# Kernel tuning notes

Measured on AMD Instinct MI355X. Metric: run time of the kernel, lower is better.

## Reference

```python
import jax, jax.numpy as jnp
import numpy as np

V, E, H, B, T = 32000, 512, 1024, 16, 256


def setup_inputs() -> dict:
    key = jax.random.key(0)
    ks = jax.random.split(key, 12)
    s = 0.05
    return {
        "x": jax.random.randint(ks[0], (B, T), 0, V),
        "emb": jax.random.normal(ks[1], (V, E), jnp.float32) * s,
        "Wx0": jax.random.normal(ks[2], (E, 3 * H), jnp.float32) * s,
        "Wh0": jax.random.normal(ks[3], (H, 3 * H), jnp.float32) * s,
        "bx0": jnp.zeros((3 * H,), jnp.float32),
        "bh0": jnp.zeros((3 * H,), jnp.float32),
        "Wx1": jax.random.normal(ks[4], (H, 3 * H), jnp.float32) * s,
        "Wh1": jax.random.normal(ks[5], (H, 3 * H), jnp.float32) * s,
        "bx1": jnp.zeros((3 * H,), jnp.float32),
        "bh1": jnp.zeros((3 * H,), jnp.float32),
        "fcW": jax.random.normal(ks[6], (H, V), jnp.float32) * s,
        "fcb": jnp.zeros((V,), jnp.float32),
    }


def _gru_cell(x_t, h, Wx, Wh, bx, bh):
    # standard torch.nn.GRUCell math
    gx = x_t @ Wx + bx            # [B, 3H]
    gh = h @ Wh + bh              # [B, 3H]
    xr, xz, xn = jnp.split(gx, 3, axis=-1)
    hr, hz, hn = jnp.split(gh, 3, axis=-1)
    r = jax.nn.sigmoid(xr + hr)
    z = jax.nn.sigmoid(xz + hz)
    n = jnp.tanh(xn + r * hn)
    return (1.0 - z) * n + z * h


def reference(x, emb, Wx0, Wh0, bx0, bh0, Wx1, Wh1, bx1, bh1, fcW, fcb):
    embedded = emb[x]                       # [B, T, E]
    xs = jnp.swapaxes(embedded, 0, 1)       # [T, B, E] for scan over time
    h0_init = jnp.zeros((x.shape[0], H), embedded.dtype)

    def step(h0, x_t):
        h0_new = _gru_cell(x_t, h0, Wx0, Wh0, bx0, bh0)
        # NOTE: original code passes h_prev = new_hidden[-1] (== layer-0 output)
        # as both input and previous hidden for layer 1. Reproduced faithfully.
        h1_new = _gru_cell(h0_new, h0_new, Wx1, Wh1, bx1, bh1)
        return h0_new, (h0_new, h1_new)

    h0_final, (h0_seq, h1_seq) = jax.lax.scan(step, h0_init, xs)
    out_seq = jnp.swapaxes(h1_seq, 0, 1)    # [B, T, H] (top-layer outputs)
    logits = out_seq @ fcW + fcb            # [B, T, V]
    h1_final = h1_seq[-1]
    hidden = jnp.stack([h0_final, h1_final], axis=0)  # [2, B, H]
    return logits, hidden
```

## Files before the change

kernel.cpp:

```cpp
#include <hip/hip_runtime.h>
#include <hip/hip_bf16.h>

#define V_  32000
#define E_  512
#define H_  1024
#define B_  16
#define T_  256
#define H3  3072

#define AGENT_LD(p)    __hip_atomic_load((p),  __ATOMIC_RELAXED, __HIP_MEMORY_SCOPE_AGENT)
#define AGENT_ST(p, v) __hip_atomic_store((p), (v), __ATOMIC_RELAXED, __HIP_MEMORY_SCOPE_AGENT)

typedef __attribute__((ext_vector_type(8))) _Float16 f16x8;
typedef __attribute__((ext_vector_type(4))) float f32x4;

#define GLDS16(gp, lp) __builtin_amdgcn_global_load_lds( \
    (const __attribute__((address_space(1))) unsigned int*)(gp), \
    (__attribute__((address_space(3))) unsigned int*)(lp), 16, 0, 0)

__global__ __launch_bounds__(128) void k_embed_f16(const int* __restrict__ x,
                                                   const float* __restrict__ emb,
                                                   _Float16* __restrict__ ef) {
  const int rin = blockIdx.x;
  const int b = rin >> 8, t = rin & 255;
  const int orow = t * 16 + b;
  const int idx = x[rin];
  const float4 v = ((const float4*)(emb + (size_t)idx * E_))[threadIdx.x];
  _Float16 o[4] = {(_Float16)v.x, (_Float16)v.y, (_Float16)v.z, (_Float16)v.w};
  ushort4 u;
  u.x = *(unsigned short*)&o[0]; u.y = *(unsigned short*)&o[1];
  u.z = *(unsigned short*)&o[2]; u.w = *(unsigned short*)&o[3];
  ((ushort4*)(ef + (size_t)orow * E_))[threadIdx.x] = u;
}

__global__ __launch_bounds__(256) void k_transpose_f16(const float* __restrict__ W, int ldw,
                                                       _Float16* __restrict__ WT, int R) {
  __shared__ float tile[32][33];
  const int c0 = blockIdx.x * 32, r0 = blockIdx.y * 32;
  const int tx = threadIdx.x & 31, ty = threadIdx.x >> 5;
  #pragma unroll
  for (int i = ty; i < 32; i += 8)
    tile[i][tx] = W[(size_t)(r0 + i) * ldw + c0 + tx];
  __syncthreads();
  #pragma unroll
  for (int i = ty; i < 32; i += 8)
    WT[(size_t)(c0 + i) * R + r0 + tx] = (_Float16)tile[tx][i];
}

__global__ __launch_bounds__(512) void k_catbias(const float* __restrict__ a,
                                                 const float* __restrict__ b,
                                                 float* __restrict__ o) {
  const int i = blockIdx.x * 512 + threadIdx.x;
  o[i] = (i < H3) ? a[i] : b[i - H3];
}

__global__ __launch_bounds__(256, 4) void k_gemm_f16(
    const _Float16* __restrict__ A, const _Float16* __restrict__ BT,
    const float* __restrict__ bias, void* __restrict__ Cv,
    int MT, int NT, int K, int ldc, int remap, int cfp16) {
  __shared__ _Float16 sA[128 * 64], sB[128 * 64];

  const int bid = blockIdx.x;
  const int GROUPM = 8;
  const int group = bid / (GROUPM * NT);
  const int first = group * GROUPM;
  const int gsm = (MT - first < GROUPM) ? (MT - first) : GROUPM;
  const int rem = bid % (GROUPM * NT);
  const int pm = first + rem % gsm;
  const int pn = rem / gsm;
  const int bm = pm * 128, bn = pn * 128;

  const int tid = threadIdx.x;
  const int wv = tid >> 6, l = tid & 63;
  const int wr = wv >> 1, wc = wv & 1;
  const int frow = l & 15;
  const int ksl  = l >> 4;

  f32x4 acc[4][4];
  #pragma unroll
  for (int a = 0; a < 4; ++a)
    #pragma unroll
    for (int b = 0; b < 4; ++b) acc[a][b] = (f32x4){0.f, 0.f, 0.f, 0.f};

  for (int k0 = 0; k0 < K; k0 += 64) {
    __syncthreads();
    #pragma unroll
    for (int p = 0; p < 4; ++p) {
      const int obase = ((p << 2) + wv) << 10;
      const int row = ((obase >> 7)) + (l >> 3);
      const int slot = l & 7;
      const int gcol = k0 + ((slot ^ (row & 7)) << 3);
      GLDS16(A + (size_t)(bm + row) * K + gcol, (char*)sA + obase);
      GLDS16(BT + (size_t)(bn + row) * K + gcol, (char*)sB + obase);
    }
    __syncthreads();
    #pragma unroll
    for (int kk = 0; kk < 2; ++kk) {
      f16x8 a[4], b[4];
      #pragma unroll
      for (int f = 0; f < 4; ++f) {
        const int ar = wr * 64 + f * 16 + frow;
        a[f] = *(const f16x8*)((const char*)sA + ar * 128 + ((((kk << 2) + ksl) ^ (ar & 7)) << 4));
        const int br_ = wc * 64 + f * 16 + frow;
        b[f] = *(const f16x8*)((const char*)sB + br_ * 128 + ((((kk << 2) + ksl) ^ (br_ & 7)) << 4));
      }
      #pragma unroll
      for (int fm = 0; fm < 4; ++fm)
        #pragma unroll
        for (int fn = 0; fn < 4; ++fn)
          acc[fm][fn] = __builtin_amdgcn_mfma_f32_16x16x32_f16(a[fm], b[fn], acc[fm][fn], 0, 0, 0);
    }
  }

  const int crow0 = bm + wr * 64 + (l >> 4) * 4;
  const int ccol0 = bn + wc * 64 + (l & 15);
  #pragma unroll
  for (int fn = 0; fn < 4; ++fn) {
    const int col = ccol0 + fn * 16;
    const float bv = bias[col];
    #pragma unroll
    for (int fm = 0; fm < 4; ++fm) {
      const int r0 = crow0 + fm * 16;
      #pragma unroll
      for (int i = 0; i < 4; ++i) {
        const int rr = r0 + i;
        const int orow = remap ? ((rr & 15) * T_ + (rr >> 4)) : rr;
        const float val = acc[fm][fn][i] + bv;
        if (cfp16) ((_Float16*)Cv)[(size_t)orow * ldc + col] = (_Float16)val;
        else       ((float*)Cv)[(size_t)orow * ldc + col] = val;
      }
    }
  }
}

__global__ __launch_bounds__(512, 1) void k_recur3(
    const _Float16* __restrict__ WhTf,
    const float* __restrict__ GX0,
    const float* __restrict__ bh0,
    _Float16* __restrict__ H0f,
    float* __restrict__ H0last,
    unsigned* __restrict__ bar,
    const float* __restrict__ Wx1,
    const float* __restrict__ Wh1,
    _Float16* __restrict__ BTf) {
  __shared__ float red[12288];
  const int tid = threadIdx.x;
  const int wg = blockIdx.x;

  if (wg >= 32) {
    float* tile = red;
    const int ty = tid >> 5, tx = tid & 31;
    for (int tix = wg - 32; tix < 6144; tix += 224) {
      const int job = tix >= 3072;
      const int tt = job ? tix - 3072 : tix;
      const int c0 = (tt % 96) * 32, r0 = (tt / 96) * 32;
      const float* W = job ? Wh1 : Wx1;
      _Float16* D = BTf + (job ? (size_t)H3 * H_ : 0);
      __syncthreads();
      tile[ty * 33 + tx]        = W[(size_t)(r0 + ty) * H3 + c0 + tx];
      tile[(ty + 16) * 33 + tx] = W[(size_t)(r0 + ty + 16) * H3 + c0 + tx];
      __syncthreads();
      #pragma unroll
      for (int s = 0; s < 2; ++s) {
        const int i = ty + s * 16;
        D[(size_t)(c0 + i) * H_ + r0 + tx] = (_Float16)tile[tx * 33 + i];
      }
    }
    return;
  }

  const int rank = wg;
  const int wv = tid >> 6, l = tid & 63;
  const int b  = tid >> 5, jj = tid & 31;
  const int col = rank * 32 + jj;

  f16x8 breg[6][4];
  #pragma unroll
  for (int nf = 0; nf < 6; ++nf) {
    const int g = nf >> 1, h2 = nf & 1;
    const int bcol = g * 1024 + rank * 32 + h2 * 16 + (l & 15);
    #pragma unroll
    for (int kf = 0; kf < 4; ++kf)
      breg[nf][kf] = *(const f16x8*)(WhTf + (size_t)bcol * 1024 + wv * 128 + kf * 32 + ((l >> 4) << 3));
  }
  const float bhr = bh0[col], bhz = bh0[1024 + col], bhn = bh0[2048 + col];

  float xr, xz, xn;
  {
    const size_t g0 = (size_t)(0 * 16 + b) * H3;
    xr = GX0[g0 + col]; xz = GX0[g0 + 1024 + col]; xn = GX0[g0 + 2048 + col];
  }
  float hprev = 0.f;

  for (int t = 0; t < T_; ++t) {
    f16x8 af[4];
    if (t == 0) {
      #pragma unroll
      for (int kf = 0; kf < 4; ++kf)
        af[kf] = (f16x8){0, 0, 0, 0, 0, 0, 0, 0};
    } else {
      const unsigned* tp = &bar[(unsigned)((4 * wv + (l & 3)) * 32 + rank) * 32];
      int guard = 0;
      for (;;) {
        const unsigned v = AGENT_LD(tp);
        if (__all(v >= (unsigned)t)) break;
        if (++guard > 10000000) break;
      }
      const char* ab = (const char*)H0f + (size_t)(t - 1) * 32768 + ((l & 15) * 2048)
                       + ((wv * 128 + ((l >> 4) << 3)) << 1);
      #pragma unroll
      for (int kf = 0; kf < 4; ++kf)
        asm volatile("global_load_dwordx4 %0, %1, off sc0 sc1" : "=v"(af[kf]) : "v"(ab + kf * 64));
      asm volatile("s_waitcnt vmcnt(0)" ::: "memory");
      __builtin_amdgcn_sched_barrier(0);
    }

    #pragma unroll
    for (int nf = 0; nf < 6; ++nf) {
      f32x4 a4 = (f32x4){0.f, 0.f, 0.f, 0.f};
      #pragma unroll
      for (int kf = 0; kf < 4; ++kf)
        a4 = __builtin_amdgcn_mfma_f32_16x16x32_f16(af[kf], breg[nf][kf], a4, 0, 0, 0);
      *(f32x4*)&red[(((wv * 6 + nf) << 6) + l) << 2] = a4;
    }
    __syncthreads();

    const int h2 = jj >> 4, f = jj & 15;
    const int lp = ((b >> 2) << 4) + f, ii = b & 3;
    float p3[3];
    #pragma unroll
    for (int g = 0; g < 3; ++g) {
      const int nf = g * 2 + h2;
      float s = 0.f;
      #pragma unroll
      for (int w8 = 0; w8 < 8; ++w8)
        s += red[((((w8 * 6 + nf) << 6) + lp) << 2) + ii];
      p3[g] = s;
    }
    const float r = 1.f / (1.f + expf(-(xr + p3[0] + bhr)));
    const float z = 1.f / (1.f + expf(-(xz + p3[1] + bhz)));
    const float n = tanhf(xn + r * (p3[2] + bhn));
    const float hnew = (1.f - z) * n + z * hprev;
    hprev = hnew;

    {
      const _Float16 hf = (_Float16)hnew;
      const unsigned tmp = (unsigned)*(const unsigned short*)&hf;
      const unsigned nb = __shfl_xor(tmp, 1);
      if ((jj & 1) == 0) {
        const unsigned w = (tmp & 0xffffu) | (nb << 16);
        const size_t u32i = (((size_t)(t * 16 + b) << 10) + col) >> 1;
        AGENT_ST((unsigned*)H0f + u32i, w);
      }
    }
    if (t == T_ - 1) H0last[(b << 10) + col] = hnew;

    if (t + 1 < T_) {
      __syncthreads();
      if (tid < 32) AGENT_ST(&bar[(unsigned)(rank * 32 + tid) * 32], (unsigned)(t + 1));
      {
        const size_t g0 = (size_t)((t + 1) * 16 + b) * H3;
        xr = GX0[g0 + col]; xz = GX0[g0 + 1024 + col]; xn = GX0[g0 + 2048 + col];
      }
    }
  }
}

__global__ __launch_bounds__(256) void k_gru1(const _Float16* __restrict__ G1f,
                                              const _Float16* __restrict__ H0f,
                                              _Float16* __restrict__ H1f,
                                              float* __restrict__ H1last, int row0) {
  const int lrow = blockIdx.x;
  const int row = row0 + lrow;
  const _Float16* g = G1f + (size_t)lrow * 6144;
  for (int j = threadIdx.x; j < H_; j += 256) {
    const float xr = (float)g[j], xz = (float)g[1024 + j], xn = (float)g[2048 + j];
    const float hr = (float)g[3072 + j], hz = (float)g[4096 + j], hn = (float)g[5120 + j];
    const size_t idx = ((size_t)row << 10) + j;
    const float h = (float)H0f[idx];
    const float r = 1.f / (1.f + expf(-(xr + hr)));
    const float z = 1.f / (1.f + expf(-(xz + hz)));
    const float n = tanhf(xn + r * hn);
    const float hnew = (1.f - z) * n + z * h;
    H1f[idx] = (_Float16)hnew;
    if (row >= 4080) H1last[((row - 4080) << 10) + j] = hnew;
  }
}

__global__ __launch_bounds__(256) void k_hidden(const float* __restrict__ H0last,
                                                const float* __restrict__ H1last,
                                                float* __restrict__ out) {
  const int i = blockIdx.x * 256 + threadIdx.x;
  const int l = i >> 14;
  const int bj = i & 16383;
  out[i] = l ? H1last[bj] : H0last[bj];
}

extern "C" void kernel_launch(void* const* d_in, const int* in_sizes, int n_in,
                              void* d_out, int out_size, void* d_ws, size_t ws_size,
                              hipStream_t stream) {
  const int*   x   = (const int*)d_in[0];
  const float* emb = (const float*)d_in[1];
  const float* Wx0 = (const float*)d_in[2];
  const float* Wh0 = (const float*)d_in[3];
  const float* bx0 = (const float*)d_in[4];
  const float* bh0 = (const float*)d_in[5];
  const float* Wx1 = (const float*)d_in[6];
  const float* Wh1 = (const float*)d_in[7];
  const float* bx1 = (const float*)d_in[8];
  const float* bh1 = (const float*)d_in[9];
  const float* fcW = (const float*)d_in[10];
  const float* fcb = (const float*)d_in[11];
  float* out = (float*)d_out;

  char* ws = (char*)d_ws;
  const size_t MB = 1024 * 1024;
  _Float16* H0f    = (_Float16*)(ws + 0);
  _Float16* H1f    = (_Float16*)(ws + 8 * MB);
  float*    H0last = (float*)(ws + 16 * MB);
  float*    H1last = (float*)(ws + 16 * MB + 65536);
  char* S = ws + 32 * MB;
  _Float16* WhTf  = (_Float16*)(S);
  float*    GX0   = (float*)(S + 8 * MB);
  _Float16* EmbF  = (_Float16*)(S + 56 * MB);
  _Float16* Wx0Tf = (_Float16*)(S + 60 * MB);
  _Float16* BTf   = (_Float16*)(S + 56 * MB);
  unsigned* bar   = (unsigned*)(S + 80 * MB);
  float*    b1cat = (float*)(S + 80 * MB + 131072);
  _Float16* G1f = (_Float16*)(S + 8 * MB);
  _Float16* fcTf = (_Float16*)(S);

  k_embed_f16<<<dim3(B_ * T_), dim3(128), 0, stream>>>(x, emb, EmbF);
  k_transpose_f16<<<dim3(H3 / 32, H_ / 32), dim3(256), 0, stream>>>(Wh0, H3, WhTf, H_);
  k_transpose_f16<<<dim3(H3 / 32, E_ / 32), dim3(256), 0, stream>>>(Wx0, H3, Wx0Tf, E_);
  k_gemm_f16<<<dim3(32 * 24), dim3(256), 0, stream>>>(
      EmbF, Wx0Tf, bx0, GX0, 32, 24, E_, H3, 0, 0);
  k_catbias<<<dim3(12), dim3(512), 0, stream>>>(bx1, bh1, b1cat);

  hipMemsetAsync(bar, 0, 131072, stream);
  {
    void* args[] = {(void*)&WhTf, (void*)&GX0, (void*)&bh0, (void*)&H0f, (void*)&H0last,
                    (void*)&bar, (void*)&Wx1, (void*)&Wh1, (void*)&BTf};
    hipLaunchCooperativeKernel((const void*)k_recur3, dim3(256), dim3(512), args, 0, stream);
  }

  for (int chunk = 0; chunk < 2; ++chunk) {
    const _Float16* Ac = H0f + (size_t)chunk * 2048 * H_;
    k_gemm_f16<<<dim3(16 * 48), dim3(256), 0, stream>>>(
        Ac, BTf, b1cat, G1f, 16, 48, H_, 6144, 0, 1);
    k_gru1<<<dim3(2048), dim3(256), 0, stream>>>(G1f, H0f, H1f, H1last, chunk * 2048);
  }

  for (int chunk = 0; chunk < 2; ++chunk) {
    const float* Wc = fcW + (size_t)chunk * 16000;
    k_transpose_f16<<<dim3(16000 / 32, H_ / 32), dim3(256), 0, stream>>>(Wc, V_, fcTf, H_);
    k_gemm_f16<<<dim3(32 * 125), dim3(256), 0, stream>>>(
        H1f, fcTf, fcb + (size_t)chunk * 16000,
        out + (size_t)chunk * 16000, 32, 125, H_, V_, 1, 0);
  }

  k_hidden<<<dim3(32768 / 256), dim3(256), 0, stream>>>(H0last, H1last,
                                                        out + (size_t)B_ * T_ * V_);
}
```

Measured before the change: 1.405 ms.

## Replace flag barrier with sentinel-polled data; overlap fc weight transpose with recurrence

New measurement: 1.401 ms. About the same (-0.3%).

```diff
diff --git a/kernel.cpp b/kernel.cpp
--- a/kernel.cpp
+++ b/kernel.cpp
@@ -8,8 +8,8 @@
 #define T_  256
 #define H3  3072
 
-#define AGENT_LD(p)    __hip_atomic_load((p),  __ATOMIC_RELAXED, __HIP_MEMORY_SCOPE_AGENT)
 #define AGENT_ST(p, v) __hip_atomic_store((p), (v), __ATOMIC_RELAXED, __HIP_MEMORY_SCOPE_AGENT)
+#define SENT 0x7F7F7F7Fu
 
 typedef __attribute__((ext_vector_type(8))) _Float16 f16x8;
 typedef __attribute__((ext_vector_type(4))) float f32x4;
@@ -139,10 +139,12 @@
     const float* __restrict__ bh0,
     _Float16* __restrict__ H0f,
     float* __restrict__ H0last,
-    unsigned* __restrict__ bar,
     const float* __restrict__ Wx1,
     const float* __restrict__ Wh1,
-    _Float16* __restrict__ BTf) {
+    _Float16* __restrict__ BTf,
+    const float* __restrict__ fcW,
+    _Float16* __restrict__ fcTf,
+    int doFC) {
   __shared__ float red[12288];
   const int tid = threadIdx.x;
   const int wg = blockIdx.x;
@@ -150,15 +152,26 @@
   if (wg >= 32) {
     float* tile = red;
     const int ty = tid >> 5, tx = tid & 31;
-    for (int tix = wg - 32; tix < 6144; tix += 224) {
-      const int job = tix >= 3072;
-      const int tt = job ? tix - 3072 : tix;
-      const int c0 = (tt % 96) * 32, r0 = (tt / 96) * 32;
-      const float* W = job ? Wh1 : Wx1;
-      _Float16* D = BTf + (job ? (size_t)H3 * H_ : 0);
+    const int total = doFC ? (6144 + 32000) : 6144;
+    for (int tix = wg - 32; tix < total; tix += 224) {
+      const float* W;
+      _Float16* D;
+      int c0, r0, ldw;
+      if (tix < 6144) {
+        const int job = tix >= 3072;
+        const int tt = job ? tix - 3072 : tix;
+        c0 = (tt % 96) * 32; r0 = (tt / 96) * 32;
+        W = job ? Wh1 : Wx1;
+        D = BTf + (job ? (size_t)H3 * H_ : 0);
+        ldw = H3;
+      } else {
+        const int tt = tix - 6144;
+        c0 = (tt % 1000) * 32; r0 = (tt / 1000) * 32;
+        W = fcW; D = fcTf; ldw = V_;
+      }
       __syncthreads();
-      tile[ty * 33 + tx]        = W[(size_t)(r0 + ty) * H3 + c0 + tx];
-      tile[(ty + 16) * 33 + tx] = W[(size_t)(r0 + ty + 16) * H3 + c0 + tx];
+      tile[ty * 33 + tx]        = W[(size_t)(r0 + ty) * ldw + c0 + tx];
+      tile[(ty + 16) * 33 + tx] = W[(size_t)(r0 + ty + 16) * ldw + c0 + tx];
       __syncthreads();
       #pragma unroll
       for (int s = 0; s < 2; ++s) {
@@ -199,19 +212,22 @@
       for (int kf = 0; kf < 4; ++kf)
         af[kf] = (f16x8){0, 0, 0, 0, 0, 0, 0, 0};
     } else {
-      const unsigned* tp = &bar[(unsigned)((4 * wv + (l & 3)) * 32 + rank) * 32];
-      int guard = 0;
-      for (;;) {
-        const unsigned v = AGENT_LD(tp);
-        if (__all(v >= (unsigned)t)) break;
-        if (++guard > 10000000) break;
-      }
       const char* ab = (const char*)H0f + (size_t)(t - 1) * 32768 + ((l & 15) * 2048)
                        + ((wv * 128 + ((l >> 4) << 3)) << 1);
-      #pragma unroll
-      for (int kf = 0; kf < 4; ++kf)
-        asm volatile("global_load_dwordx4 %0, %1, off sc0 sc1" : "=v"(af[kf]) : "v"(ab + kf * 64));
-      asm volatile("s_waitcnt vmcnt(0)" ::: "memory");
+      int guard = 0;
+      bool ok;
+      do {
+        #pragma unroll
+        for (int kf = 0; kf < 4; ++kf)
+          asm volatile("global_load_dwordx4 %0, %1, off sc0 sc1" : "=v"(af[kf]) : "v"(ab + kf * 64));
+        asm volatile("s_waitcnt vmcnt(0)" ::: "memory");
+        ok = true;
+        #pragma unroll
+        for (int kf = 0; kf < 4; ++kf) {
+          const uint4 u = *(const uint4*)&af[kf];
+          ok = ok && (u.x != SENT) && (u.y != SENT) && (u.z != SENT) && (u.w != SENT);
+        }
+      } while (!__all(ok) && ++guard < 10000000);
       __builtin_amdgcn_sched_barrier(0);
     }
 
@@ -257,7 +273,6 @@
 
     if (t + 1 < T_) {
       __syncthreads();
-      if (tid < 32) AGENT_ST(&bar[(unsigned)(rank * 32 + tid) * 32], (unsigned)(t + 1));
       {
         const size_t g0 = (size_t)((t + 1) * 16 + b) * H3;
         xr = GX0[g0 + col]; xz = GX0[g0 + 1024 + col]; xn = GX0[g0 + 2048 + col];
@@ -325,10 +340,12 @@
   _Float16* EmbF  = (_Float16*)(S + 56 * MB);
   _Float16* Wx0Tf = (_Float16*)(S + 60 * MB);
   _Float16* BTf   = (_Float16*)(S + 56 * MB);
-  unsigned* bar   = (unsigned*)(S + 80 * MB);
-  float*    b1cat = (float*)(S + 80 * MB + 131072);
+  float*    b1cat = (float*)(S + 80 * MB);
+  _Float16* fcTfB = (_Float16*)(S + 82 * MB);
   _Float16* G1f = (_Float16*)(S + 8 * MB);
-  _Float16* fcTf = (_Float16*)(S);
+  _Float16* fcTf1 = (_Float16*)(S);
+
+  const int doFC = (ws_size >= (size_t)190 * MB) ? 1 : 0;
 
   k_embed_f16<<<dim3(B_ * T_), dim3(128), 0, stream>>>(x, emb, EmbF);
   k_transpose_f16<<<dim3(H3 / 32, H_ / 32), dim3(256), 0, stream>>>(Wh0, H3, WhTf, H_);
@@ -337,10 +354,11 @@
       EmbF, Wx0Tf, bx0, GX0, 32, 24, E_, H3, 0, 0);
   k_catbias<<<dim3(12), dim3(512), 0, stream>>>(bx1, bh1, b1cat);
 
-  hipMemsetAsync(bar, 0, 131072, stream);
+  hipMemsetAsync(H0f, 0x7F, 8 * MB, stream);
   {
     void* args[] = {(void*)&WhTf, (void*)&GX0, (void*)&bh0, (void*)&H0f, (void*)&H0last,
-                    (void*)&bar, (void*)&Wx1, (void*)&Wh1, (void*)&BTf};
+                    (void*)&Wx1, (void*)&Wh1, (void*)&BTf,
+                    (void*)&fcW, (void*)&fcTfB, (void*)&doFC};
     hipLaunchCooperativeKernel((const void*)k_recur3, dim3(256), dim3(512), args, 0, stream);
   }
 
@@ -351,12 +369,17 @@
     k_gru1<<<dim3(2048), dim3(256), 0, stream>>>(G1f, H0f, H1f, H1last, chunk * 2048);
   }
 
-  for (int chunk = 0; chunk < 2; ++chunk) {
-    const float* Wc = fcW + (size_t)chunk * 16000;
-    k_transpose_f16<<<dim3(16000 / 32, H_ / 32), dim3(256), 0, stream>>>(Wc, V_, fcTf, H_);
-    k_gemm_f16<<<dim3(32 * 125), dim3(256), 0, stream>>>(
-        H1f, fcTf, fcb + (size_t)chunk * 16000,
-        out + (size_t)chunk * 16000, 32, 125, H_, V_, 1, 0);
+  if (doFC) {
+    k_gemm_f16<<<dim3(32 * 250), dim3(256), 0, stream>>>(
+        H1f, fcTfB, fcb, out, 32, 250, H_, V_, 1, 0);
+  } else {
+    for (int chunk = 0; chunk < 2; ++chunk) {
+      const float* Wc = fcW + (size_t)chunk * 16000;
+      k_transpose_f16<<<dim3(16000 / 32, H_ / 32), dim3(256), 0, stream>>>(Wc, V_, fcTf1, H_);
+      k_gemm_f16<<<dim3(32 * 125), dim3(256), 0, stream>>>(
+          H1f, fcTf1, fcb + (size_t)chunk * 16000,
+          out + (size_t)chunk * 16000, 32, 125, H_, V_, 1, 0);
+    }
   }
 
   k_hidden<<<dim3(32768 / 256), dim3(256), 0, stream>>>(H0last, H1last,
```
